# Optimization experiments

Measured on AMD Instinct MI355X. Metric: run time of the kernel, lower is better.

## Reference

```python
import jax, jax.numpy as jnp
import numpy as np

HEAD_DIM = 64  # hidden_dim 1024 // heads_num 16


def setup_inputs() -> dict:
    key = jax.random.key(0)
    ks = jax.random.split(key, 5)
    B, S, H = 2, 4096, 1024
    std = 1.0 / np.sqrt(H)
    return {
        "x": jax.random.normal(ks[0], (B, S, H), jnp.float32),
        "Wq": jax.random.normal(ks[1], (H, H), jnp.float32) * std,
        "bq": jnp.zeros((H,), jnp.float32),
        "Wk": jax.random.normal(ks[2], (H, H), jnp.float32) * std,
        "bk": jnp.zeros((H,), jnp.float32),
        "Wv": jax.random.normal(ks[3], (H, H), jnp.float32) * std,
        "bv": jnp.zeros((H,), jnp.float32),
        "Wo": jax.random.normal(ks[4], (H, H), jnp.float32) * std,
        "bo": jnp.zeros((H,), jnp.float32),
    }


def reference(x, Wq, bq, Wk, bk, Wv, bv, Wo, bo):
    # Linear projections (torch Linear: x @ W^T + b)
    q = jnp.einsum("bsh,oh->bso", x, Wq) + bq
    k = jnp.einsum("bsh,oh->bso", x, Wk) + bk
    v = jnp.einsum("bsh,oh->bso", x, Wv) + bv
    # all_to_all is identity on a single device (world size 1)
    scale = jnp.float32(HEAD_DIM) ** 0.5
    # Faithful to source: attention over the FULL hidden dim (no head split),
    # full [B, S, S] score matrix.
    scores = jnp.einsum("bqh,bkh->bqk", q, k) / scale
    weights = jax.nn.softmax(scores, axis=-1)
    attn = jnp.einsum("bqk,bkh->bqh", weights, v)
    out = jnp.einsum("bsh,oh->bso", attn, Wo) + bo
    return out
```

## Files before the change

### kernel.cpp

```cpp
#include <hip/hip_runtime.h>
#include <stdint.h>


typedef __bf16 bf16x8 __attribute__((ext_vector_type(8)));
typedef float  f32x4  __attribute__((ext_vector_type(4)));

__device__ __forceinline__ unsigned short f32_to_bf16_rne(float f) {
    uint32_t u = __builtin_bit_cast(uint32_t, f);
    uint32_t r = (u + 0x7FFFu + ((u >> 16) & 1u)) >> 16;
    return (unsigned short)r;
}

__global__ __launch_bounds__(256) void cvt_f32_bf16(
    const float* __restrict__ x, unsigned short* __restrict__ y, int n)
{
    int i = (blockIdx.x * 256 + threadIdx.x) * 4;
    if (i < n) {
        float4 v = *(const float4*)(x + i);
        ushort4 o;
        o.x = f32_to_bf16_rne(v.x);
        o.y = f32_to_bf16_rne(v.y);
        o.z = f32_to_bf16_rne(v.z);
        o.w = f32_to_bf16_rne(v.w);
        *(ushort4*)(y + i) = o;
    }
}

#define BM 128
#define BN 128
#define BK 64

template <int MODE>
__global__ __launch_bounds__(256) void gemm_bt(
    const unsigned short* __restrict__ A,
    const unsigned short* __restrict__ Bt,
    void* __restrict__ C, void* __restrict__ C2,
    const float* __restrict__ b0, const float* __restrict__ b1,
    const float* __restrict__ b2, float* __restrict__ rowsum,
    float alpha, int M, int N, int K,
    long long aZ, long long bZ, long long cZ)
{
    __shared__ unsigned short ldsA[BM * BK];
    __shared__ unsigned short ldsB[BN * BK];

    int G  = gridDim.x * gridDim.y * gridDim.z;
    int l  = blockIdx.x + gridDim.x * (blockIdx.y + gridDim.y * blockIdx.z);
    int mb, nb, zb;
    if ((G & 7) == 0) {
        int perx = G >> 3;
        int idx  = (l & 7) * perx + (l >> 3);
        int NB = gridDim.x, Z = gridDim.z;
        mb = idx / (NB * Z);
        int rem = idx - mb * (NB * Z);
        zb = rem / NB;
        nb = rem - zb * NB;
    } else {
        mb = blockIdx.y; nb = blockIdx.x; zb = blockIdx.z;
    }

    const unsigned short* Ab = A  + (size_t)zb * aZ;
    const unsigned short* Bb = Bt + (size_t)zb * bZ;

    const int tid  = threadIdx.x;
    const int lane = tid & 63;
    const int wave = tid >> 6;
    const int quad = lane >> 4;
    const int l16  = lane & 15;
    const int wr   = wave >> 1;
    const int wc   = wave & 1;

    const int mBase = mb * BM;
    const int nBase = nb * BN;

    f32x4 acc[4][4] = {};

    for (int k0 = 0; k0 < K; k0 += BK) {
        #pragma unroll
        for (int i = 0; i < 4; ++i) {
            int base = (i * 4 + wave) * 64;
            int s    = base + lane;
            int row  = s >> 3;
            int col  = ((s ^ (s >> 3)) & 7) * 8;
            __builtin_amdgcn_global_load_lds(
                (const __attribute__((address_space(1))) void*)(Ab + (size_t)(mBase + row) * K + (size_t)(k0 + col)),
                (__attribute__((address_space(3))) void*)(&ldsA[base * 8]),
                16, 0, 0);
        }
        #pragma unroll
        for (int i = 0; i < 4; ++i) {
            int base = (i * 4 + wave) * 64;
            int s    = base + lane;
            int row  = s >> 3;
            int col  = ((s ^ (s >> 3)) & 7) * 8;
            __builtin_amdgcn_global_load_lds(
                (const __attribute__((address_space(1))) void*)(Bb + (size_t)(nBase + row) * K + (size_t)(k0 + col)),
                (__attribute__((address_space(3))) void*)(&ldsB[base * 8]),
                16, 0, 0);
        }
        __syncthreads();

        #pragma unroll
        for (int kk = 0; kk < 2; ++kk) {
            bf16x8 af[4], bfv[4];
            #pragma unroll
            for (int mi = 0; mi < 4; ++mi) {
                int r = wr * 64 + mi * 16 + l16;
                int c = kk * 4 + quad;
                af[mi] = *(const bf16x8*)(&ldsA[r * BK + (((c ^ r) & 7) << 3)]);
            }
            #pragma unroll
            for (int ni = 0; ni < 4; ++ni) {
                int r = wc * 64 + ni * 16 + l16;
                int c = kk * 4 + quad;
                bfv[ni] = *(const bf16x8*)(&ldsB[r * BK + (((c ^ r) & 7) << 3)]);
            }
            #pragma unroll
            for (int mi = 0; mi < 4; ++mi)
                #pragma unroll
                for (int ni = 0; ni < 4; ++ni)
                    acc[mi][ni] = __builtin_amdgcn_mfma_f32_16x16x32_bf16(
                        af[mi], bfv[ni], acc[mi][ni], 0, 0, 0);
        }
        __syncthreads();
    }

    if (MODE == 0) {
        float* Cz = (float*)C;
        #pragma unroll
        for (int mi = 0; mi < 4; ++mi)
            #pragma unroll
            for (int ni = 0; ni < 4; ++ni) {
                int col = nBase + wc * 64 + ni * 16 + l16;
                float b = b0[col];
                #pragma unroll
                for (int r = 0; r < 4; ++r) {
                    int row = mBase + wr * 64 + mi * 16 + quad * 4 + r;
                    Cz[(size_t)row * N + col] = acc[mi][ni][r] + b;
                }
            }
    } else if (MODE == 3) {
        unsigned short* Pz = (unsigned short*)C + (size_t)zb * cZ;
        float* rs = rowsum + (size_t)zb * M;
        #pragma unroll
        for (int mi = 0; mi < 4; ++mi) {
            #pragma unroll
            for (int r = 0; r < 4; ++r) {
                int row = mBase + wr * 64 + mi * 16 + quad * 4 + r;
                float e[4];
                float partial = 0.f;
                #pragma unroll
                for (int ni = 0; ni < 4; ++ni) {
                    e[ni] = __expf(acc[mi][ni][r] * alpha);
                    partial += e[ni];
                }
                #pragma unroll
                for (int ni = 0; ni < 4; ++ni) {
                    int col = nBase + wc * 64 + ni * 16 + l16;
                    Pz[(size_t)row * N + col] = f32_to_bf16_rne(e[ni]);
                }
                #pragma unroll
                for (int off = 1; off < 16; off <<= 1)
                    partial += __shfl_xor(partial, off, 64);
                if (l16 == 0) atomicAdd(&rs[row], partial);
            }
        }
    } else if (MODE == 4) {
        unsigned short* Cz = (unsigned short*)C + (size_t)zb * cZ;
        const float* rs = rowsum + (size_t)zb * M;
        #pragma unroll
        for (int mi = 0; mi < 4; ++mi) {
            #pragma unroll
            for (int r = 0; r < 4; ++r) {
                int row = mBase + wr * 64 + mi * 16 + quad * 4 + r;
                float inv = 1.f / rs[row];
                #pragma unroll
                for (int ni = 0; ni < 4; ++ni) {
                    int col = nBase + wc * 64 + ni * 16 + l16;
                    Cz[(size_t)row * N + col] = f32_to_bf16_rne(acc[mi][ni][r] * inv);
                }
            }
        }
    } else {
        const float* bias = (zb == 0) ? b0 : (zb == 1) ? b1 : b2;
        #pragma unroll
        for (int mi = 0; mi < 4; ++mi)
            #pragma unroll
            for (int ni = 0; ni < 4; ++ni) {
                int col = nBase + wc * 64 + ni * 16 + l16;
                float b = bias[col];
                #pragma unroll
                for (int r = 0; r < 4; ++r) {
                    int row = mBase + wr * 64 + mi * 16 + quad * 4 + r;
                    float v = acc[mi][ni][r] + b;
                    if (zb < 2) {
                        ((unsigned short*)C)[(size_t)zb * cZ + (size_t)row * N + col] =
                            f32_to_bf16_rne(v);
                    } else {
                        int bb = row >> 12;
                        int s  = row & 4095;
                        ((unsigned short*)C2)[(size_t)bb * ((size_t)N * 4096) + (size_t)col * 4096 + s] =
                            f32_to_bf16_rne(v);
                    }
                }
            }
    }
}

extern "C" void kernel_launch(void* const* d_in, const int* in_sizes, int n_in,
                              void* d_out, int out_size, void* d_ws, size_t ws_size,
                              hipStream_t stream)
{
    const float* x  = (const float*)d_in[0];
    const float* Wq = (const float*)d_in[1];
    const float* bq = (const float*)d_in[2];
    const float* Wk = (const float*)d_in[3];
    const float* bk = (const float*)d_in[4];
    const float* Wv = (const float*)d_in[5];
    const float* bv = (const float*)d_in[6];
    const float* Wo = (const float*)d_in[7];
    const float* bo = (const float*)d_in[8];
    float* out = (float*)d_out;

    const int Bsz = 2, S = 4096, H = 1024;
    const int M = Bsz * S;

    char* p = (char*)d_ws;
    auto alloc = [&](size_t bytes) -> char* {
        char* r = p; p += (bytes + 255) & ~(size_t)255; return r;
    };
    unsigned short* wq16 = (unsigned short*)alloc((size_t)H * H * 2);
    unsigned short* wk16 = (unsigned short*)alloc((size_t)H * H * 2);
    unsigned short* wv16 = (unsigned short*)alloc((size_t)H * H * 2);
    unsigned short* wo16 = (unsigned short*)alloc((size_t)H * H * 2);
    unsigned short* q16  = (unsigned short*)alloc((size_t)M * H * 2);
    unsigned short* k16  = (unsigned short*)alloc((size_t)M * H * 2);
    unsigned short* vt16 = (unsigned short*)alloc((size_t)Bsz * H * S * 2);
    float*          rsum = (float*)alloc((size_t)Bsz * S * 4);
    char* region = alloc((size_t)Bsz * S * S * 2);
    unsigned short* p16 = (unsigned short*)region;
    unsigned short* x16 = (unsigned short*)region;
    unsigned short* a16 = q16;

    (void)wk16; (void)wv16;

    hipMemsetAsync(rsum, 0, (size_t)Bsz * S * 4, stream);

    cvt_f32_bf16<<<(M * H) / 1024, 256, 0, stream>>>(x,  x16,  M * H);
    cvt_f32_bf16<<<(H * H) / 1024, 256, 0, stream>>>(Wq, wq16, H * H);
    cvt_f32_bf16<<<(H * H) / 1024, 256, 0, stream>>>(Wk, wk16, H * H);
    cvt_f32_bf16<<<(H * H) / 1024, 256, 0, stream>>>(Wv, wv16, H * H);
    cvt_f32_bf16<<<(H * H) / 1024, 256, 0, stream>>>(Wo, wo16, H * H);

    dim3 blk(256);

    gemm_bt<5><<<dim3(H / BN, M / BM, 3), blk, 0, stream>>>(
        x16, wq16, q16, vt16, bq, bk, bv, nullptr, 1.f, M, H, H,
        0, (long long)H * H, (long long)M * H);

    gemm_bt<3><<<dim3(S / BN, S / BM, 2), blk, 0, stream>>>(
        q16, k16, p16, nullptr, nullptr, nullptr, nullptr, rsum, 0.125f,
        S, S, H, (long long)S * H, (long long)S * H, (long long)S * S);

    gemm_bt<4><<<dim3(H / BN, S / BM, 2), blk, 0, stream>>>(
        p16, vt16, a16, nullptr, nullptr, nullptr, nullptr, rsum, 1.f,
        S, H, S, (long long)S * S, (long long)H * S, (long long)S * H);

    gemm_bt<0><<<dim3(H / BN, M / BM, 1), blk, 0, stream>>>(
        a16, wo16, out, nullptr, bo, nullptr, nullptr, nullptr, 1.f,
        M, H, H, 0, 0, 0);
}
```

Baseline: 409.0 us.

## Switch GEMMs to 32x32x16 MFMA and fuse weight conversion with rowsum zeroing

Each wave's 64x64 subtile now uses four 32x32x16 bf16 MFMA accumulators instead of sixteen 16x16x32 ones. This cuts LDS fragment loads per MFMA and the instruction count. All epilogues are remapped to the 32x32 output register layout, and the softmax row reduction now spans 32 lanes. Separately, the four weight conversions and the rowsum memset are merged into one launch, reducing launch overhead.

```diff
diff --git a/kernel.cpp b/kernel.cpp
--- a/kernel.cpp
+++ b/kernel.cpp
@@ -2,8 +2,8 @@
 #include <stdint.h>
 
 
-typedef __bf16 bf16x8 __attribute__((ext_vector_type(8)));
-typedef float  f32x4  __attribute__((ext_vector_type(4)));
+typedef __bf16 bf16x8  __attribute__((ext_vector_type(8)));
+typedef float  f32x16  __attribute__((ext_vector_type(16)));
 
 __device__ __forceinline__ unsigned short f32_to_bf16_rne(float f) {
     uint32_t u = __builtin_bit_cast(uint32_t, f);
@@ -24,6 +24,29 @@
         o.w = f32_to_bf16_rne(v.w);
         *(ushort4*)(y + i) = o;
     }
+}
+
+__global__ __launch_bounds__(256) void cvt_weights(
+    const float* __restrict__ w0, const float* __restrict__ w1,
+    const float* __restrict__ w2, const float* __restrict__ w3,
+    unsigned short* __restrict__ dst, float* __restrict__ rsum)
+{
+    int b = blockIdx.x;
+    if (b >= 4096) {
+        int i = ((b - 4096) * 256 + threadIdx.x) * 4;
+        *(float4*)(rsum + i) = float4{0.f, 0.f, 0.f, 0.f};
+        return;
+    }
+    int which = b >> 10;
+    const float* src = which == 0 ? w0 : which == 1 ? w1 : which == 2 ? w2 : w3;
+    int i = ((b & 1023) * 256 + threadIdx.x) * 4;
+    float4 v = *(const float4*)(src + i);
+    ushort4 o;
+    o.x = f32_to_bf16_rne(v.x);
+    o.y = f32_to_bf16_rne(v.y);
+    o.z = f32_to_bf16_rne(v.z);
+    o.w = f32_to_bf16_rne(v.w);
+    *(ushort4*)(dst + (size_t)which * 1048576 + i) = o;
 }
 
 #define BM 128
@@ -64,15 +87,15 @@
     const int tid  = threadIdx.x;
     const int lane = tid & 63;
     const int wave = tid >> 6;
-    const int quad = lane >> 4;
-    const int l16  = lane & 15;
+    const int l32  = lane & 31;
+    const int half = lane >> 5;
     const int wr   = wave >> 1;
     const int wc   = wave & 1;
 
     const int mBase = mb * BM;
     const int nBase = nb * BN;
 
-    f32x4 acc[4][4] = {};
+    f32x16 acc[2][2] = {};
 
     for (int k0 = 0; k0 < K; k0 += BK) {
         #pragma unroll
@@ -100,25 +123,24 @@
         __syncthreads();
 
         #pragma unroll
-        for (int kk = 0; kk < 2; ++kk) {
-            bf16x8 af[4], bfv[4];
-            #pragma unroll
-            for (int mi = 0; mi < 4; ++mi) {
-                int r = wr * 64 + mi * 16 + l16;
-                int c = kk * 4 + quad;
+        for (int t = 0; t < 4; ++t) {
+            int c = t * 2 + half;
+            bf16x8 af[2], bfv[2];
+            #pragma unroll
+            for (int mi = 0; mi < 2; ++mi) {
+                int r = wr * 64 + mi * 32 + l32;
                 af[mi] = *(const bf16x8*)(&ldsA[r * BK + (((c ^ r) & 7) << 3)]);
             }
             #pragma unroll
-            for (int ni = 0; ni < 4; ++ni) {
-                int r = wc * 64 + ni * 16 + l16;
-                int c = kk * 4 + quad;
+            for (int ni = 0; ni < 2; ++ni) {
+                int r = wc * 64 + ni * 32 + l32;
                 bfv[ni] = *(const bf16x8*)(&ldsB[r * BK + (((c ^ r) & 7) << 3)]);
             }
             #pragma unroll
-            for (int mi = 0; mi < 4; ++mi)
-                #pragma unroll
-                for (int ni = 0; ni < 4; ++ni)
-                    acc[mi][ni] = __builtin_amdgcn_mfma_f32_16x16x32_bf16(
+            for (int mi = 0; mi < 2; ++mi)
+                #pragma unroll
+                for (int ni = 0; ni < 2; ++ni)
+                    acc[mi][ni] = __builtin_amdgcn_mfma_f32_32x32x16_bf16(
                         af[mi], bfv[ni], acc[mi][ni], 0, 0, 0);
         }
         __syncthreads();
@@ -127,71 +149,67 @@
     if (MODE == 0) {
         float* Cz = (float*)C;
         #pragma unroll
-        for (int mi = 0; mi < 4; ++mi)
-            #pragma unroll
-            for (int ni = 0; ni < 4; ++ni) {
-                int col = nBase + wc * 64 + ni * 16 + l16;
+        for (int mi = 0; mi < 2; ++mi)
+            #pragma unroll
+            for (int ni = 0; ni < 2; ++ni) {
+                int col = nBase + wc * 64 + ni * 32 + l32;
                 float b = b0[col];
                 #pragma unroll
-                for (int r = 0; r < 4; ++r) {
-                    int row = mBase + wr * 64 + mi * 16 + quad * 4 + r;
-                    Cz[(size_t)row * N + col] = acc[mi][ni][r] + b;
+                for (int reg = 0; reg < 16; ++reg) {
+                    int row = mBase + wr * 64 + mi * 32 + (reg & 3) + 8 * (reg >> 2) + 4 * half;
+                    Cz[(size_t)row * N + col] = acc[mi][ni][reg] + b;
                 }
             }
     } else if (MODE == 3) {
         unsigned short* Pz = (unsigned short*)C + (size_t)zb * cZ;
         float* rs = rowsum + (size_t)zb * M;
         #pragma unroll
-        for (int mi = 0; mi < 4; ++mi) {
-            #pragma unroll
-            for (int r = 0; r < 4; ++r) {
-                int row = mBase + wr * 64 + mi * 16 + quad * 4 + r;
-                float e[4];
+        for (int mi = 0; mi < 2; ++mi) {
+            #pragma unroll
+            for (int reg = 0; reg < 16; ++reg) {
+                int row = mBase + wr * 64 + mi * 32 + (reg & 3) + 8 * (reg >> 2) + 4 * half;
                 float partial = 0.f;
                 #pragma unroll
-                for (int ni = 0; ni < 4; ++ni) {
-                    e[ni] = __expf(acc[mi][ni][r] * alpha);
-                    partial += e[ni];
-                }
-                #pragma unroll
-                for (int ni = 0; ni < 4; ++ni) {
-                    int col = nBase + wc * 64 + ni * 16 + l16;
-                    Pz[(size_t)row * N + col] = f32_to_bf16_rne(e[ni]);
-                }
-                #pragma unroll
-                for (int off = 1; off < 16; off <<= 1)
+                for (int ni = 0; ni < 2; ++ni) {
+                    float e = __expf(acc[mi][ni][reg] * alpha);
+                    partial += e;
+                    int col = nBase + wc * 64 + ni * 32 + l32;
+                    Pz[(size_t)row * N + col] = f32_to_bf16_rne(e);
+                }
+                #pragma unroll
+                for (int off = 1; off < 32; off <<= 1)
                     partial += __shfl_xor(partial, off, 64);
-                if (l16 == 0) atomicAdd(&rs[row], partial);
+                if (l32 == 0) atomicAdd(&rs[row], partial);
             }
         }
     } else if (MODE == 4) {
         unsigned short* Cz = (unsigned short*)C + (size_t)zb * cZ;
         const float* rs = rowsum + (size_t)zb * M;
         #pragma unroll
-        for (int mi = 0; mi < 4; ++mi) {
-            #pragma unroll
-            for (int r = 0; r < 4; ++r) {
-                int row = mBase + wr * 64 + mi * 16 + quad * 4 + r;
+        for (int mi = 0; mi < 2; ++mi) {
+            #pragma unroll
+            for (int reg = 0; reg < 16; ++reg) {
+                int row = mBase + wr * 64 + mi * 32 + (reg & 3) + 8 * (reg >> 2) + 4 * half;
                 float inv = 1.f / rs[row];
                 #pragma unroll
-                for (int ni = 0; ni < 4; ++ni) {
-                    int col = nBase + wc * 64 + ni * 16 + l16;
-                    Cz[(size_t)row * N + col] = f32_to_bf16_rne(acc[mi][ni][r] * inv);
+                for (int ni = 0; ni < 2; ++ni) {
+                    int col = nBase + wc * 64 + ni * 32 + l32;
+                    Cz[(size_t)row * N + col] = f32_to_bf16_rne(acc[mi][ni][reg] * inv);
                 }
             }
         }
     } else {
         const float* bias = (zb == 0) ? b0 : (zb == 1) ? b1 : b2;
         #pragma unroll
-        for (int mi = 0; mi < 4; ++mi)
-            #pragma unroll
-            for (int ni = 0; ni < 4; ++ni) {
-                int col = nBase + wc * 64 + ni * 16 + l16;
+        for (int mi = 0; mi < 2; ++mi)
+            #pragma unroll
+            for (int ni = 0; ni < 2; ++ni) {
+                int col = nBase + wc * 64 + ni * 32 + l32;
                 float b = bias[col];
                 #pragma unroll
-                for (int r = 0; r < 4; ++r) {
-                    int row = mBase + wr * 64 + mi * 16 + quad * 4 + r;
-                    float v = acc[mi][ni][r] + b;
+                for (int reg = 0; reg < 16; ++reg) {
+                    int row = mBase + wr * 64 + mi * 32 + (reg & 3) + 8 * (reg >> 2) + 4 * half;
+                    float v = acc[mi][ni][reg] + b;
                     if (zb < 2) {
                         ((unsigned short*)C)[(size_t)zb * cZ + (size_t)row * N + col] =
                             f32_to_bf16_rne(v);
@@ -228,10 +246,11 @@
     auto alloc = [&](size_t bytes) -> char* {
         char* r = p; p += (bytes + 255) & ~(size_t)255; return r;
     };
-    unsigned short* wq16 = (unsigned short*)alloc((size_t)H * H * 2);
-    unsigned short* wk16 = (unsigned short*)alloc((size_t)H * H * 2);
-    unsigned short* wv16 = (unsigned short*)alloc((size_t)H * H * 2);
-    unsigned short* wo16 = (unsigned short*)alloc((size_t)H * H * 2);
+    unsigned short* w16  = (unsigned short*)alloc((size_t)4 * H * H * 2);
+    unsigned short* wq16 = w16;
+    unsigned short* wk16 = w16 + (size_t)1 * H * H;
+    unsigned short* wv16 = w16 + (size_t)2 * H * H;
+    unsigned short* wo16 = w16 + (size_t)3 * H * H;
     unsigned short* q16  = (unsigned short*)alloc((size_t)M * H * 2);
     unsigned short* k16  = (unsigned short*)alloc((size_t)M * H * 2);
     unsigned short* vt16 = (unsigned short*)alloc((size_t)Bsz * H * S * 2);
@@ -241,15 +260,8 @@
     unsigned short* x16 = (unsigned short*)region;
     unsigned short* a16 = q16;
 
-    (void)wk16; (void)wv16;
-
-    hipMemsetAsync(rsum, 0, (size_t)Bsz * S * 4, stream);
-
-    cvt_f32_bf16<<<(M * H) / 1024, 256, 0, stream>>>(x,  x16,  M * H);
-    cvt_f32_bf16<<<(H * H) / 1024, 256, 0, stream>>>(Wq, wq16, H * H);
-    cvt_f32_bf16<<<(H * H) / 1024, 256, 0, stream>>>(Wk, wk16, H * H);
-    cvt_f32_bf16<<<(H * H) / 1024, 256, 0, stream>>>(Wv, wv16, H * H);
-    cvt_f32_bf16<<<(H * H) / 1024, 256, 0, stream>>>(Wo, wo16, H * H);
+    cvt_f32_bf16<<<(M * H) / 1024, 256, 0, stream>>>(x, x16, M * H);
+    cvt_weights<<<4096 + 8, 256, 0, stream>>>(Wq, Wk, Wv, Wo, w16, rsum);
 
     dim3 blk(256);
 
```

New measurement: 409.6 us. No clear change (+0.1%).

## Fold output projection into V and fuse normalization with output bias

Applied to the files above, without the earlier changes.

Reassociates (P·V)·Wo^T as P·(V·Wo^T) by computing Wo·V^T per batch, so the PV GEMM writes the final float output with row normalization and output bias applied, and the separate output-projection GEMM is dropped. V is now stored untransposed, and a new small GEMM produces the transposed V·Wo^T product. The four weight conversions and the rowsum zeroing are merged into one launch. The extra GEMM has the same FLOPs as the removed one, so the savings come from fewer launches, no separate attention-output round trip, and coalesced V stores. The cost is one more rounding to bf16 of V·Wo^T before the attention product, which shifts numerical error.

```diff
diff --git a/kernel.cpp b/kernel.cpp
--- a/kernel.cpp
+++ b/kernel.cpp
@@ -24,6 +24,29 @@
         o.w = f32_to_bf16_rne(v.w);
         *(ushort4*)(y + i) = o;
     }
+}
+
+__global__ __launch_bounds__(256) void cvt_weights(
+    const float* __restrict__ w0, const float* __restrict__ w1,
+    const float* __restrict__ w2, const float* __restrict__ w3,
+    unsigned short* __restrict__ dst, float* __restrict__ rsum)
+{
+    int b = blockIdx.x;
+    if (b >= 4096) {
+        int i = ((b - 4096) * 256 + threadIdx.x) * 4;
+        *(float4*)(rsum + i) = float4{0.f, 0.f, 0.f, 0.f};
+        return;
+    }
+    int which = b >> 10;
+    const float* src = which == 0 ? w0 : which == 1 ? w1 : which == 2 ? w2 : w3;
+    int i = ((b & 1023) * 256 + threadIdx.x) * 4;
+    float4 v = *(const float4*)(src + i);
+    ushort4 o;
+    o.x = f32_to_bf16_rne(v.x);
+    o.y = f32_to_bf16_rne(v.y);
+    o.z = f32_to_bf16_rne(v.z);
+    o.w = f32_to_bf16_rne(v.w);
+    *(ushort4*)(dst + (size_t)which * 1048576 + i) = o;
 }
 
 #define BM 128
@@ -124,18 +147,18 @@
         __syncthreads();
     }
 
-    if (MODE == 0) {
-        float* Cz = (float*)C;
+    if (MODE == 1) {
+        unsigned short* Cz = (unsigned short*)C + (size_t)zb * cZ;
         #pragma unroll
         for (int mi = 0; mi < 4; ++mi)
             #pragma unroll
             for (int ni = 0; ni < 4; ++ni) {
                 int col = nBase + wc * 64 + ni * 16 + l16;
-                float b = b0[col];
+                float b = b0 ? b0[col] : 0.f;
                 #pragma unroll
                 for (int r = 0; r < 4; ++r) {
                     int row = mBase + wr * 64 + mi * 16 + quad * 4 + r;
-                    Cz[(size_t)row * N + col] = acc[mi][ni][r] + b;
+                    Cz[(size_t)row * N + col] = f32_to_bf16_rne(acc[mi][ni][r] + b);
                 }
             }
     } else if (MODE == 3) {
@@ -164,8 +187,24 @@
                 if (l16 == 0) atomicAdd(&rs[row], partial);
             }
         }
-    } else if (MODE == 4) {
-        unsigned short* Cz = (unsigned short*)C + (size_t)zb * cZ;
+    } else if (MODE == 5) {
+        const float* bias = (zb == 0) ? b0 : (zb == 1) ? b1 : b2;
+        unsigned short* Cz = (zb < 2) ? ((unsigned short*)C + (size_t)zb * cZ)
+                                      : (unsigned short*)C2;
+        #pragma unroll
+        for (int mi = 0; mi < 4; ++mi)
+            #pragma unroll
+            for (int ni = 0; ni < 4; ++ni) {
+                int col = nBase + wc * 64 + ni * 16 + l16;
+                float b = bias[col];
+                #pragma unroll
+                for (int r = 0; r < 4; ++r) {
+                    int row = mBase + wr * 64 + mi * 16 + quad * 4 + r;
+                    Cz[(size_t)row * N + col] = f32_to_bf16_rne(acc[mi][ni][r] + b);
+                }
+            }
+    } else {
+        float* Cz = (float*)C + (size_t)zb * cZ;
         const float* rs = rowsum + (size_t)zb * M;
         #pragma unroll
         for (int mi = 0; mi < 4; ++mi) {
@@ -176,33 +215,10 @@
                 #pragma unroll
                 for (int ni = 0; ni < 4; ++ni) {
                     int col = nBase + wc * 64 + ni * 16 + l16;
-                    Cz[(size_t)row * N + col] = f32_to_bf16_rne(acc[mi][ni][r] * inv);
-                }
-            }
-        }
-    } else {
-        const float* bias = (zb == 0) ? b0 : (zb == 1) ? b1 : b2;
-        #pragma unroll
-        for (int mi = 0; mi < 4; ++mi)
-            #pragma unroll
-            for (int ni = 0; ni < 4; ++ni) {
-                int col = nBase + wc * 64 + ni * 16 + l16;
-                float b = bias[col];
-                #pragma unroll
-                for (int r = 0; r < 4; ++r) {
-                    int row = mBase + wr * 64 + mi * 16 + quad * 4 + r;
-                    float v = acc[mi][ni][r] + b;
-                    if (zb < 2) {
-                        ((unsigned short*)C)[(size_t)zb * cZ + (size_t)row * N + col] =
-                            f32_to_bf16_rne(v);
-                    } else {
-                        int bb = row >> 12;
-                        int s  = row & 4095;
-                        ((unsigned short*)C2)[(size_t)bb * ((size_t)N * 4096) + (size_t)col * 4096 + s] =
-                            f32_to_bf16_rne(v);
-                    }
-                }
-            }
+                    Cz[(size_t)row * N + col] = acc[mi][ni][r] * inv + b0[col];
+                }
+            }
+        }
     }
 }
 
@@ -228,44 +244,36 @@
     auto alloc = [&](size_t bytes) -> char* {
         char* r = p; p += (bytes + 255) & ~(size_t)255; return r;
     };
-    unsigned short* wq16 = (unsigned short*)alloc((size_t)H * H * 2);
-    unsigned short* wk16 = (unsigned short*)alloc((size_t)H * H * 2);
-    unsigned short* wv16 = (unsigned short*)alloc((size_t)H * H * 2);
-    unsigned short* wo16 = (unsigned short*)alloc((size_t)H * H * 2);
+    unsigned short* w16  = (unsigned short*)alloc((size_t)4 * H * H * 2);
+    unsigned short* wq16 = w16;
+    unsigned short* wo16 = w16 + (size_t)3 * H * H;
     unsigned short* q16  = (unsigned short*)alloc((size_t)M * H * 2);
     unsigned short* k16  = (unsigned short*)alloc((size_t)M * H * 2);
-    unsigned short* vt16 = (unsigned short*)alloc((size_t)Bsz * H * S * 2);
+    unsigned short* vot16= (unsigned short*)alloc((size_t)Bsz * H * S * 2);
     float*          rsum = (float*)alloc((size_t)Bsz * S * 4);
     char* region = alloc((size_t)Bsz * S * S * 2);
+    unsigned short* x16 = (unsigned short*)region;
+    unsigned short* v16 = (unsigned short*)region + (size_t)M * H;
     unsigned short* p16 = (unsigned short*)region;
-    unsigned short* x16 = (unsigned short*)region;
-    unsigned short* a16 = q16;
-
-    (void)wk16; (void)wv16;
-
-    hipMemsetAsync(rsum, 0, (size_t)Bsz * S * 4, stream);
-
-    cvt_f32_bf16<<<(M * H) / 1024, 256, 0, stream>>>(x,  x16,  M * H);
-    cvt_f32_bf16<<<(H * H) / 1024, 256, 0, stream>>>(Wq, wq16, H * H);
-    cvt_f32_bf16<<<(H * H) / 1024, 256, 0, stream>>>(Wk, wk16, H * H);
-    cvt_f32_bf16<<<(H * H) / 1024, 256, 0, stream>>>(Wv, wv16, H * H);
-    cvt_f32_bf16<<<(H * H) / 1024, 256, 0, stream>>>(Wo, wo16, H * H);
+
+    cvt_f32_bf16<<<(M * H) / 1024, 256, 0, stream>>>(x, x16, M * H);
+    cvt_weights<<<4096 + 8, 256, 0, stream>>>(Wq, Wk, Wv, Wo, w16, rsum);
 
     dim3 blk(256);
 
     gemm_bt<5><<<dim3(H / BN, M / BM, 3), blk, 0, stream>>>(
-        x16, wq16, q16, vt16, bq, bk, bv, nullptr, 1.f, M, H, H,
+        x16, wq16, q16, v16, bq, bk, bv, nullptr, 1.f, M, H, H,
         0, (long long)H * H, (long long)M * H);
+
+    gemm_bt<1><<<dim3(S / BN, H / BM, 2), blk, 0, stream>>>(
+        wo16, v16, vot16, nullptr, nullptr, nullptr, nullptr, nullptr, 1.f,
+        H, S, H, 0, (long long)S * H, (long long)H * S);
 
     gemm_bt<3><<<dim3(S / BN, S / BM, 2), blk, 0, stream>>>(
         q16, k16, p16, nullptr, nullptr, nullptr, nullptr, rsum, 0.125f,
         S, S, H, (long long)S * H, (long long)S * H, (long long)S * S);
 
-    gemm_bt<4><<<dim3(H / BN, S / BM, 2), blk, 0, stream>>>(
-        p16, vt16, a16, nullptr, nullptr, nullptr, nullptr, rsum, 1.f,
+    gemm_bt<6><<<dim3(H / BN, S / BM, 2), blk, 0, stream>>>(
+        p16, vot16, out, nullptr, bo, nullptr, nullptr, rsum, 1.f,
         S, H, S, (long long)S * S, (long long)H * S, (long long)S * H);
-
-    gemm_bt<0><<<dim3(H / BN, M / BM, 1), blk, 0, stream>>>(
-        a16, wo16, out, nullptr, bo, nullptr, nullptr, nullptr, 1.f,
-        M, H, H, 0, 0, 0);
-}
+}
```

Result: faster. 387.0 us (-5.4%).
